# Kernel optimization log

Hardware: AMD Instinct MI355X
Metric: run time of the kernel (lower is better)

The kernel has to match this reference:

```python
import jax, jax.numpy as jnp
import numpy as np

HIDDEN = 1024
FEAT = 64
BATCH = 512
SEQ = 64
EPS = 1e-5


def _gru_layer(x_seq, Wih, Whh, bih, bhh):
    # x_seq: [B,T,Din]; Wih: [3H,Din]; Whh: [3H,H]; gate order r,z,n (PyTorch)
    B = x_seq.shape[0]
    H = Whh.shape[1]
    gates_x = jnp.einsum('btd,gd->btg', x_seq, Wih) + bih  # [B,T,3H]
    h0 = jnp.zeros((B, H), x_seq.dtype)

    def step(h, gx):
        gh = h @ Whh.T + bhh                       # [B,3H]
        xr, xz, xn = jnp.split(gx, 3, axis=-1)
        hr, hz, hn = jnp.split(gh, 3, axis=-1)
        r = jax.nn.sigmoid(xr + hr)
        z = jax.nn.sigmoid(xz + hz)
        n = jnp.tanh(xn + r * hn)
        h_new = (1.0 - z) * n + z * h
        return h_new, h_new

    _, ys = jax.lax.scan(step, h0, jnp.swapaxes(gates_x, 0, 1))  # [T,B,H]
    return jnp.swapaxes(ys, 0, 1)                                # [B,T,H]


def setup_inputs() -> dict:
    key = jax.random.key(0)
    ks = jax.random.split(key, 20)
    s = 1.0 / np.sqrt(HIDDEN)
    u = lambda k, shape: jax.random.uniform(k, shape, jnp.float32, -s, s)
    inp = {
        'x': jax.random.normal(ks[0], (BATCH, SEQ, FEAT), jnp.float32),
        'Wih0': u(ks[1], (3 * HIDDEN, FEAT)),
        'Whh0': u(ks[2], (3 * HIDDEN, HIDDEN)),
        'bih0': u(ks[3], (3 * HIDDEN,)),
        'bhh0': u(ks[4], (3 * HIDDEN,)),
        'Wih1': u(ks[5], (3 * HIDDEN, HIDDEN)),
        'Whh1': u(ks[6], (3 * HIDDEN, HIDDEN)),
        'bih1': u(ks[7], (3 * HIDDEN,)),
        'bhh1': u(ks[8], (3 * HIDDEN,)),
        'Wih2': u(ks[9], (3 * HIDDEN, HIDDEN)),
        'Whh2': u(ks[10], (3 * HIDDEN, HIDDEN)),
        'bih2': u(ks[11], (3 * HIDDEN,)),
        'bhh2': u(ks[12], (3 * HIDDEN,)),
        'gamma': jnp.ones((HIDDEN,), jnp.float32),
        'beta': jnp.zeros((HIDDEN,), jnp.float32),
        'fcW': u(ks[13], (1, HIDDEN)),
        'fcb': u(ks[14], (1,)),
    }
    return inp


def reference(x, Wih0, Whh0, bih0, bhh0, Wih1, Whh1, bih1, bhh1,
              Wih2, Whh2, bih2, bhh2, gamma, beta, fcW, fcb):
    h = _gru_layer(x, Wih0, Whh0, bih0, bhh0)
    h = _gru_layer(h, Wih1, Whh1, bih1, bhh1)
    h = _gru_layer(h, Wih2, Whh2, bih2, bhh2)
    out = h[:, -1, :]                               # [B,H] last timestep
    # BatchNorm1d in training mode: biased batch stats (B != 1 branch)
    mu = jnp.mean(out, axis=0)
    var = jnp.mean((out - mu) ** 2, axis=0)
    out = (out - mu) * jax.lax.rsqrt(var + EPS) * gamma + beta
    out = out @ fcW.T + fcb                         # [B,1]
    return jax.nn.sigmoid(out)[:, 0]                # [B]
```

## Files before the change

### kernel.cpp

```cpp
#include <hip/hip_runtime.h>
#include <hip/hip_bf16.h>
#include <stdint.h>

#define HIDDEN 1024
#define FEAT   64
#define BATCH  512
#define SEQ    64
#define GATES  3072

typedef __attribute__((ext_vector_type(4))) float f32x4;
typedef __attribute__((ext_vector_type(8))) short s16x8;

#define MFMA16(a, b, c) __builtin_amdgcn_mfma_f32_16x16x32_bf16(a, b, c, 0, 0, 0)
#define VMCNT(n) asm volatile("s_waitcnt vmcnt(" #n ")" ::: "memory")
#define LGKMCNT0 asm volatile("s_waitcnt lgkmcnt(0)" ::: "memory")

__device__ inline unsigned short f2bf(float f) {
    unsigned u = __builtin_bit_cast(unsigned, f);
    u += 0x7fff + ((u >> 16) & 1);
    return (unsigned short)(u >> 16);
}
__device__ inline float bf2f(unsigned short s) {
    unsigned u = ((unsigned)s) << 16;
    return __builtin_bit_cast(float, u);
}

#define GLOAD_LDS16(g, l) __builtin_amdgcn_global_load_lds( \
    (const __attribute__((address_space(1))) unsigned int*)(g), \
    (__attribute__((address_space(3))) unsigned int*)(l), 16, 0, 0)

__global__ void k_conv_whh_t(const float* __restrict__ src, unsigned short* __restrict__ dst) {
    int i = blockIdx.x * 256 + threadIdx.x;
    int ub = i / 98304;
    int r  = i - ub * 98304;
    int c  = r / 6144;
    int r2 = r - c * 6144;
    int srow = r2 >> 6, scol = r2 & 63;
    int ug = srow / 48, rr = srow - ug * 48;
    int g = rr >> 4, jj = rr & 15;
    int src_row = (g << 10) + (ub << 5) + (ug << 4) + jj;
    dst[i] = f2bf(src[(size_t)src_row * 1024 + (c << 6) + scol]);
}

__global__ void k_conv_wih0_t(const float* __restrict__ src, unsigned short* __restrict__ dst) {
    int i = blockIdx.x * 256 + threadIdx.x;
    int ub = i / 6144;
    int r  = i - ub * 6144;
    int srow = r >> 6, scol = r & 63;
    int ug = srow / 48, rr = srow - ug * 48;
    int g = rr >> 4, jj = rr & 15;
    int src_row = (g << 10) + (ub << 5) + (ug << 4) + jj;
    dst[i] = f2bf(src[(size_t)src_row * 64 + scol]);
}

__global__ void k_xpose(const float* __restrict__ x, unsigned short* __restrict__ xbf) {
    int i = blockIdx.x * blockDim.x + threadIdx.x;
    if (i >= BATCH * SEQ * FEAT) return;
    int f = i & 63, t = (i >> 6) & 63, b = i >> 12;
    xbf[((size_t)t * BATCH + b) * FEAT + f] = f2bf(x[i]);
}

__device__ __forceinline__ void stage_pair(const char* ws, const char* as,
                                           unsigned short* Wd, unsigned short* Ad,
                                           int wid, int lane)
{
    const int lrow = lane >> 3;
    const int srcoff = lrow * 128 + (((lane & 7) ^ (lrow & 7)) << 4);
#pragma unroll
    for (int r = 0; r < 3; ++r) {
        int g = wid * 3 + r;
        GLOAD_LDS16(ws + (g << 10) + srcoff, (char*)Wd + (g << 10));
    }
#pragma unroll
    for (int r = 0; r < 4; ++r) {
        int g = wid + r * 4;
        GLOAD_LDS16(as + (g << 10) + srcoff, (char*)Ad + (g << 10));
    }
}

template<int NSLOT>
__device__ __forceinline__ void compute_chunk(const unsigned short* aL, const unsigned short* wL,
                                              int wid, int lane, f32x4 (&acc)[2][2][4])
{
    const int l15 = lane & 15, hi = lane >> 4;
    const int swz = (l15 & 7) << 4;
    const char* ap = (const char*)aL;
    const char* wp = (const char*)wL;
#pragma unroll
    for (int ks = 0; ks < 2; ++ks) {
        const int kb = ks * 64 + (hi << 4);
        s16x8 a0 = *(const s16x8*)(ap + ((((wid * 32 + l15) * 128) + kb) ^ swz));
        s16x8 a1 = *(const s16x8*)(ap + ((((wid * 32 + 16 + l15) * 128) + kb) ^ swz));
#pragma unroll
        for (int ug = 0; ug < 2; ++ug) {
            const int wr = ug * 48 + l15;
            s16x8 b0 = *(const s16x8*)(wp + ((((wr)      * 128) + kb) ^ swz));
            s16x8 b1 = *(const s16x8*)(wp + ((((wr + 16) * 128) + kb) ^ swz));
            s16x8 b2 = *(const s16x8*)(wp + ((((wr + 32) * 128) + kb) ^ swz));
            acc[0][ug][0]     = MFMA16(a0, b0, acc[0][ug][0]);
            acc[0][ug][1]     = MFMA16(a0, b1, acc[0][ug][1]);
            acc[0][ug][NSLOT] = MFMA16(a0, b2, acc[0][ug][NSLOT]);
            acc[1][ug][0]     = MFMA16(a1, b0, acc[1][ug][0]);
            acc[1][ug][1]     = MFMA16(a1, b1, acc[1][ug][1]);
            acc[1][ug][NSLOT] = MFMA16(a1, b2, acc[1][ug][NSLOT]);
        }
    }
}

__global__ __launch_bounds__(256, 2) void k_stage(
    int d,
    const unsigned short* __restrict__ xbf,
    unsigned short* __restrict__ h0,
    unsigned short* __restrict__ h1,
    unsigned short* __restrict__ h2,
    const unsigned short* __restrict__ wih0R,
    const unsigned short* __restrict__ whh0R,
    const unsigned short* __restrict__ wih1R,
    const unsigned short* __restrict__ whh1R,
    const unsigned short* __restrict__ wih2R,
    const unsigned short* __restrict__ whh2R,
    const float* __restrict__ bih0, const float* __restrict__ bhh0,
    const float* __restrict__ bih1, const float* __restrict__ bhh1,
    const float* __restrict__ bih2, const float* __restrict__ bhh2)
{
    __shared__ unsigned short Wb[2][96 * 64];
    __shared__ unsigned short Ab[2][128 * 64];
    const int bid = blockIdx.x;
    const int slot = bid & 7;
    const int p = (bid >> 3) % 12;
    const int bg = bid / 96;
    const int pair = slot + 8 * p;
    const int layer = pair >> 5;
    const int ub = pair & 31;
    const int t = d - layer;
    if (t < 0 || t >= SEQ) return;

    const int tid = threadIdx.x;
    const int wid = tid >> 6, lane = tid & 63;
    const int l15 = lane & 15, hi = lane >> 4;
    const int brow0 = bg * 128;

    const unsigned short* inseq = (layer == 0) ? xbf : ((layer == 1) ? h0 : h1);
    unsigned short* outseq = (layer == 0) ? h0 : ((layer == 1) ? h1 : h2);
    const unsigned short* wihR = (layer == 0) ? wih0R : ((layer == 1) ? wih1R : wih2R);
    const unsigned short* whhR = (layer == 0) ? whh0R : ((layer == 1) ? whh1R : whh2R);

    const char* a1base = (layer == 0)
        ? (const char*)xbf + (size_t)t * 65536 + (size_t)brow0 * 128
        : (const char*)inseq + (size_t)(t & 1) * 1048576 + (size_t)brow0 * 128;
    const char* w1base = (layer == 0)
        ? (const char*)wih0R + (size_t)ub * 12288
        : (const char*)wihR + (size_t)ub * 196608;
    const char* a2base = (const char*)outseq + (size_t)((t - 1) & 1) * 1048576 + (size_t)brow0 * 128;
    const char* w2base = (const char*)whhR + (size_t)ub * 196608;

    const int NCH1 = (layer == 0) ? 1 : 16;
    const int NCH2 = (t > 0) ? 16 : 0;
    const int total = NCH1 + NCH2;

    auto srcs = [&](int c, const char*& ws, const char*& as) {
        if (c < NCH1) {
            ws = w1base + (size_t)c * 12288;
            as = a1base + (size_t)c * 65536;
        } else {
            int c2 = c - NCH1;
            ws = w2base + (size_t)c2 * 12288;
            as = a2base + (size_t)c2 * 65536;
        }
    };

    f32x4 acc[2][2][4];
    const f32x4 zero = {0.f, 0.f, 0.f, 0.f};
#pragma unroll
    for (int i = 0; i < 2; ++i)
#pragma unroll
        for (int ug = 0; ug < 2; ++ug)
#pragma unroll
            for (int s = 0; s < 4; ++s) acc[i][ug][s] = zero;

    {
        const char* ws; const char* as;
        srcs(0, ws, as);
        stage_pair(ws, as, Wb[0], Ab[0], wid, lane);
    }

    for (int c = 0; c < total; ++c) {
        const int cb = c & 1;
        if (c + 1 < total) {
            const char* ws; const char* as;
            srcs(c + 1, ws, as);
            stage_pair(ws, as, Wb[cb ^ 1], Ab[cb ^ 1], wid, lane);
            VMCNT(7);
        } else {
            VMCNT(0);
        }
        __builtin_amdgcn_s_barrier();
        __builtin_amdgcn_sched_barrier(0);
        if (c < NCH1) compute_chunk<2>(Ab[cb], Wb[cb], wid, lane, acc);
        else          compute_chunk<3>(Ab[cb], Wb[cb], wid, lane, acc);
        LGKMCNT0;
        __builtin_amdgcn_sched_barrier(0);
        __builtin_amdgcn_s_barrier();
    }

    const float* bih = (layer == 0) ? bih0 : ((layer == 1) ? bih1 : bih2);
    const float* bhh = (layer == 0) ? bhh0 : ((layer == 1) ? bhh1 : bhh2);
    const unsigned short* hprev = outseq + (size_t)((t > 0) ? ((t - 1) & 1) : 0) * (512 * 1024);
    unsigned short* hout = outseq + (size_t)(t & 1) * (512 * 1024);
    const int jc = ub >> 1;
#pragma unroll
    for (int ug = 0; ug < 2; ++ug) {
        const int j = ub * 32 + ug * 16 + l15;
        const int jcol = (ub & 1) * 32 + ug * 16 + l15;
        const float br  = bih[j] + bhh[j];
        const float bz  = bih[HIDDEN + j] + bhh[HIDDEN + j];
        const float bxn = bih[2 * HIDDEN + j];
        const float bhn = bhh[2 * HIDDEN + j];
#pragma unroll
        for (int i = 0; i < 2; ++i)
#pragma unroll
            for (int r = 0; r < 4; ++r) {
                int brow = brow0 + wid * 32 + i * 16 + hi * 4 + r;
                size_t hidx = (size_t)(jc * 512 + brow) * 64 + jcol;
                float rg = 1.f / (1.f + __expf(-(acc[i][ug][0][r] + br)));
                float zg = 1.f / (1.f + __expf(-(acc[i][ug][1][r] + bz)));
                float ng = tanhf(acc[i][ug][2][r] + bxn + rg * (acc[i][ug][3][r] + bhn));
                float hv = (t > 0) ? bf2f(hprev[hidx]) : 0.f;
                float hnew = (1.f - zg) * ng + zg * hv;
                hout[hidx] = f2bf(hnew);
            }
    }
}

__global__ void k_bn_part(const unsigned short* __restrict__ h, float* __restrict__ part) {
    int j = threadIdx.x;
    int blk = blockIdx.x;
    const int jc = j >> 6, jcol = j & 63;
    float s = 0.f, q = 0.f;
    for (int b = blk * 32; b < blk * 32 + 32; ++b) {
        float v = bf2f(h[(size_t)(jc * 512 + b) * 64 + jcol]);
        s += v; q += v * v;
    }
    part[blk * 2048 + j] = s;
    part[blk * 2048 + 1024 + j] = q;
}

__global__ void k_bn_fold(const float* __restrict__ part, const float* __restrict__ gamma,
                          const float* __restrict__ beta, float* __restrict__ a, float* __restrict__ bb)
{
    int j = blockIdx.x * 256 + threadIdx.x;
    float s = 0.f, q = 0.f;
    for (int p = 0; p < 16; ++p) {
        s += part[p * 2048 + j];
        q += part[p * 2048 + 1024 + j];
    }
    float mu = s * (1.f / BATCH);
    float var = q * (1.f / BATCH) - mu * mu;
    float rs = rsqrtf(var + 1e-5f);
    float aj = gamma[j] * rs;
    a[j] = aj;
    bb[j] = beta[j] - mu * aj;
}

__global__ void k_fc(const unsigned short* __restrict__ h, const float* __restrict__ a, const float* __restrict__ bb,
                     const float* __restrict__ fcW, const float* __restrict__ fcb, float* __restrict__ out)
{
    int b = blockIdx.x;
    int lane = threadIdx.x;
    float s = 0.f;
    for (int j = lane; j < HIDDEN; j += 64)
        s += (bf2f(h[(size_t)((j >> 6) * 512 + b) * 64 + (j & 63)]) * a[j] + bb[j]) * fcW[j];
#pragma unroll
    for (int m = 32; m; m >>= 1) s += __shfl_xor(s, m, 64);
    if (lane == 0) out[b] = 1.f / (1.f + __expf(-(s + fcb[0])));
}

extern "C" void kernel_launch(void* const* d_in, const int* in_sizes, int n_in,
                              void* d_out, int out_size, void* d_ws, size_t ws_size,
                              hipStream_t stream)
{
    const float* x = (const float*)d_in[0];
    const float* W_ih[3] = {(const float*)d_in[1], (const float*)d_in[5], (const float*)d_in[9]};
    const float* W_hh[3] = {(const float*)d_in[2], (const float*)d_in[6], (const float*)d_in[10]};
    const float* b_ih[3] = {(const float*)d_in[3], (const float*)d_in[7], (const float*)d_in[11]};
    const float* b_hh[3] = {(const float*)d_in[4], (const float*)d_in[8], (const float*)d_in[12]};
    const float* gamma = (const float*)d_in[13];
    const float* beta  = (const float*)d_in[14];
    const float* fcW   = (const float*)d_in[15];
    const float* fcb   = (const float*)d_in[16];

    char* ws = (char*)d_ws;
    size_t off = 0;
    auto alloc = [&](size_t bytes) -> void* {
        void* p = ws + off;
        off = (off + bytes + 255) & ~(size_t)255;
        return p;
    };
    unsigned short* wih0R = (unsigned short*)alloc((size_t)GATES * FEAT * 2);
    unsigned short* whh0R = (unsigned short*)alloc((size_t)GATES * HIDDEN * 2);
    unsigned short* wih1R = (unsigned short*)alloc((size_t)GATES * HIDDEN * 2);
    unsigned short* whh1R = (unsigned short*)alloc((size_t)GATES * HIDDEN * 2);
    unsigned short* wih2R = (unsigned short*)alloc((size_t)GATES * HIDDEN * 2);
    unsigned short* whh2R = (unsigned short*)alloc((size_t)GATES * HIDDEN * 2);
    unsigned short* xbf = (unsigned short*)alloc((size_t)SEQ * BATCH * FEAT * 2);
    unsigned short* h0  = (unsigned short*)alloc((size_t)2 * BATCH * HIDDEN * 2);
    unsigned short* h1  = (unsigned short*)alloc((size_t)2 * BATCH * HIDDEN * 2);
    unsigned short* h2  = (unsigned short*)alloc((size_t)2 * BATCH * HIDDEN * 2);
    float* part = (float*)alloc(16 * 2048 * 4);
    float* abuf = (float*)alloc(HIDDEN * 4);
    float* bbuf = (float*)alloc(HIDDEN * 4);

    k_conv_wih0_t<<<(GATES * FEAT) / 256, 256, 0, stream>>>(W_ih[0], wih0R);
    k_conv_whh_t<<<(GATES * HIDDEN) / 256, 256, 0, stream>>>(W_hh[0], whh0R);
    k_conv_whh_t<<<(GATES * HIDDEN) / 256, 256, 0, stream>>>(W_ih[1], wih1R);
    k_conv_whh_t<<<(GATES * HIDDEN) / 256, 256, 0, stream>>>(W_hh[1], whh1R);
    k_conv_whh_t<<<(GATES * HIDDEN) / 256, 256, 0, stream>>>(W_ih[2], wih2R);
    k_conv_whh_t<<<(GATES * HIDDEN) / 256, 256, 0, stream>>>(W_hh[2], whh2R);
    k_xpose<<<(BATCH * SEQ * FEAT + 255) / 256, 256, 0, stream>>>(x, xbf);

    for (int d = 0; d < SEQ + 2; ++d)
        k_stage<<<384, 256, 0, stream>>>(d, xbf, h0, h1, h2,
                                         wih0R, whh0R, wih1R, whh1R, wih2R, whh2R,
                                         b_ih[0], b_hh[0], b_ih[1], b_hh[1], b_ih[2], b_hh[2]);

    const unsigned short* hlast = h2 + (size_t)((SEQ - 1) & 1) * (BATCH * HIDDEN);
    k_bn_part<<<16, 1024, 0, stream>>>(hlast, part);
    k_bn_fold<<<HIDDEN / 256, 256, 0, stream>>>(part, gamma, beta, abuf, bbuf);
    k_fc<<<BATCH, 64, 0, stream>>>(hlast, abuf, bbuf, fcW, fcb, (float*)d_out);
}
```

Baseline: 2.530 ms.

## Halve batch tile per block to 64 rows, doubling grid to 768 blocks

Each block now covers 64 batch rows instead of 128, so each wave computes one 16-row MFMA tile rather than two, and the per-step grid doubles to 768 blocks. Launch bounds move to 3 blocks per CU, and MFMA sections are wrapped in s_setprio. The aim is more parallelism and better CU fill for the latency-bound wavefront step, at the price of each block reloading the same weight tiles, which doubles weight traffic. The diff also adds an unused whhR alias that now points at wih2R for layer 2, which looks like stray editing.

```diff
diff --git a/kernel.cpp b/kernel.cpp
--- a/kernel.cpp
+++ b/kernel.cpp
@@ -72,7 +72,7 @@
         GLOAD_LDS16(ws + (g << 10) + srcoff, (char*)Wd + (g << 10));
     }
 #pragma unroll
-    for (int r = 0; r < 4; ++r) {
+    for (int r = 0; r < 2; ++r) {
         int g = wid + r * 4;
         GLOAD_LDS16(as + (g << 10) + srcoff, (char*)Ad + (g << 10));
     }
@@ -80,34 +80,32 @@
 
 template<int NSLOT>
 __device__ __forceinline__ void compute_chunk(const unsigned short* aL, const unsigned short* wL,
-                                              int wid, int lane, f32x4 (&acc)[2][2][4])
+                                              int wid, int lane, f32x4 (&acc)[2][4])
 {
     const int l15 = lane & 15, hi = lane >> 4;
     const int swz = (l15 & 7) << 4;
     const char* ap = (const char*)aL;
     const char* wp = (const char*)wL;
+    __builtin_amdgcn_s_setprio(1);
 #pragma unroll
     for (int ks = 0; ks < 2; ++ks) {
         const int kb = ks * 64 + (hi << 4);
-        s16x8 a0 = *(const s16x8*)(ap + ((((wid * 32 + l15) * 128) + kb) ^ swz));
-        s16x8 a1 = *(const s16x8*)(ap + ((((wid * 32 + 16 + l15) * 128) + kb) ^ swz));
+        s16x8 a0 = *(const s16x8*)(ap + ((((wid * 16 + l15) * 128) + kb) ^ swz));
 #pragma unroll
         for (int ug = 0; ug < 2; ++ug) {
             const int wr = ug * 48 + l15;
             s16x8 b0 = *(const s16x8*)(wp + ((((wr)      * 128) + kb) ^ swz));
             s16x8 b1 = *(const s16x8*)(wp + ((((wr + 16) * 128) + kb) ^ swz));
             s16x8 b2 = *(const s16x8*)(wp + ((((wr + 32) * 128) + kb) ^ swz));
-            acc[0][ug][0]     = MFMA16(a0, b0, acc[0][ug][0]);
-            acc[0][ug][1]     = MFMA16(a0, b1, acc[0][ug][1]);
-            acc[0][ug][NSLOT] = MFMA16(a0, b2, acc[0][ug][NSLOT]);
-            acc[1][ug][0]     = MFMA16(a1, b0, acc[1][ug][0]);
-            acc[1][ug][1]     = MFMA16(a1, b1, acc[1][ug][1]);
-            acc[1][ug][NSLOT] = MFMA16(a1, b2, acc[1][ug][NSLOT]);
+            acc[ug][0]     = MFMA16(a0, b0, acc[ug][0]);
+            acc[ug][1]     = MFMA16(a0, b1, acc[ug][1]);
+            acc[ug][NSLOT] = MFMA16(a0, b2, acc[ug][NSLOT]);
         }
     }
-}
-
-__global__ __launch_bounds__(256, 2) void k_stage(
+    __builtin_amdgcn_s_setprio(0);
+}
+
+__global__ __launch_bounds__(256, 3) void k_stage(
     int d,
     const unsigned short* __restrict__ xbf,
     unsigned short* __restrict__ h0,
@@ -124,7 +122,7 @@
     const float* __restrict__ bih2, const float* __restrict__ bhh2)
 {
     __shared__ unsigned short Wb[2][96 * 64];
-    __shared__ unsigned short Ab[2][128 * 64];
+    __shared__ unsigned short Ab[2][64 * 64];
     const int bid = blockIdx.x;
     const int slot = bid & 7;
     const int p = (bid >> 3) % 12;
@@ -138,12 +136,13 @@
     const int tid = threadIdx.x;
     const int wid = tid >> 6, lane = tid & 63;
     const int l15 = lane & 15, hi = lane >> 4;
-    const int brow0 = bg * 128;
+    const int brow0 = bg * 64;
 
     const unsigned short* inseq = (layer == 0) ? xbf : ((layer == 1) ? h0 : h1);
     unsigned short* outseq = (layer == 0) ? h0 : ((layer == 1) ? h1 : h2);
     const unsigned short* wihR = (layer == 0) ? wih0R : ((layer == 1) ? wih1R : wih2R);
-    const unsigned short* whhR = (layer == 0) ? whh0R : ((layer == 1) ? whh1R : whh2R);
+    const unsigned short* whhR = (layer == 0) ? whh0R : ((layer == 1) ? whh1R : wih2R);
+    const unsigned short* whhRx = (layer == 0) ? whh0R : ((layer == 1) ? whh1R : whh2R);
 
     const char* a1base = (layer == 0)
         ? (const char*)xbf + (size_t)t * 65536 + (size_t)brow0 * 128
@@ -152,7 +151,7 @@
         ? (const char*)wih0R + (size_t)ub * 12288
         : (const char*)wihR + (size_t)ub * 196608;
     const char* a2base = (const char*)outseq + (size_t)((t - 1) & 1) * 1048576 + (size_t)brow0 * 128;
-    const char* w2base = (const char*)whhR + (size_t)ub * 196608;
+    const char* w2base = (const char*)whhRx + (size_t)ub * 196608;
 
     const int NCH1 = (layer == 0) ? 1 : 16;
     const int NCH2 = (t > 0) ? 16 : 0;
@@ -169,14 +168,12 @@
         }
     };
 
-    f32x4 acc[2][2][4];
+    f32x4 acc[2][4];
     const f32x4 zero = {0.f, 0.f, 0.f, 0.f};
 #pragma unroll
-    for (int i = 0; i < 2; ++i)
-#pragma unroll
-        for (int ug = 0; ug < 2; ++ug)
-#pragma unroll
-            for (int s = 0; s < 4; ++s) acc[i][ug][s] = zero;
+    for (int ug = 0; ug < 2; ++ug)
+#pragma unroll
+        for (int s = 0; s < 4; ++s) acc[ug][s] = zero;
 
     {
         const char* ws; const char* as;
@@ -190,7 +187,7 @@
             const char* ws; const char* as;
             srcs(c + 1, ws, as);
             stage_pair(ws, as, Wb[cb ^ 1], Ab[cb ^ 1], wid, lane);
-            VMCNT(7);
+            VMCNT(5);
         } else {
             VMCNT(0);
         }
@@ -217,18 +214,16 @@
         const float bxn = bih[2 * HIDDEN + j];
         const float bhn = bhh[2 * HIDDEN + j];
 #pragma unroll
-        for (int i = 0; i < 2; ++i)
-#pragma unroll
-            for (int r = 0; r < 4; ++r) {
-                int brow = brow0 + wid * 32 + i * 16 + hi * 4 + r;
-                size_t hidx = (size_t)(jc * 512 + brow) * 64 + jcol;
-                float rg = 1.f / (1.f + __expf(-(acc[i][ug][0][r] + br)));
-                float zg = 1.f / (1.f + __expf(-(acc[i][ug][1][r] + bz)));
-                float ng = tanhf(acc[i][ug][2][r] + bxn + rg * (acc[i][ug][3][r] + bhn));
-                float hv = (t > 0) ? bf2f(hprev[hidx]) : 0.f;
-                float hnew = (1.f - zg) * ng + zg * hv;
-                hout[hidx] = f2bf(hnew);
-            }
+        for (int r = 0; r < 4; ++r) {
+            int brow = brow0 + wid * 16 + hi * 4 + r;
+            size_t hidx = (size_t)(jc * 512 + brow) * 64 + jcol;
+            float rg = 1.f / (1.f + __expf(-(acc[ug][0][r] + br)));
+            float zg = 1.f / (1.f + __expf(-(acc[ug][1][r] + bz)));
+            float ng = tanhf(acc[ug][2][r] + bxn + rg * (acc[ug][3][r] + bhn));
+            float hv = (t > 0) ? bf2f(hprev[hidx]) : 0.f;
+            float hnew = (1.f - zg) * ng + zg * hv;
+            hout[hidx] = f2bf(hnew);
+        }
     }
 }
 
@@ -319,7 +314,7 @@
     k_xpose<<<(BATCH * SEQ * FEAT + 255) / 256, 256, 0, stream>>>(x, xbf);
 
     for (int d = 0; d < SEQ + 2; ++d)
-        k_stage<<<384, 256, 0, stream>>>(d, xbf, h0, h1, h2,
+        k_stage<<<768, 256, 0, stream>>>(d, xbf, h0, h1, h2,
                                          wih0R, whh0R, wih1R, whh1R, wih2R, whh2R,
                                          b_ih[0], b_hh[0], b_ih[1], b_hh[1], b_ih[2], b_hh[2]);
 
```

After: 2.032 ms. 1.25x faster.
